# Kernel optimization log

Hardware: AMD Instinct MI355X
Metric: run time of the kernel (lower is better)

The kernel has to match this reference:

```python
import jax, jax.numpy as jnp
import numpy as np

H, W, D = 1024, 1024, 128


def setup_inputs() -> dict:
    key = jax.random.key(0)
    ks = jax.random.split(key, 7)
    x = jax.random.normal(ks[0], (2, H, W), dtype=jnp.float32)
    s1 = 1.0 / np.sqrt(4.0)
    s2 = 1.0 / np.sqrt(float(D))
    W1 = jax.random.uniform(ks[1], (4, D), jnp.float32, -s1, s1)
    b1 = jax.random.uniform(ks[2], (D,), jnp.float32, -s1, s1)
    W2 = jax.random.uniform(ks[3], (D, D), jnp.float32, -s2, s2)
    b2 = jax.random.uniform(ks[4], (D,), jnp.float32, -s2, s2)
    W3 = jax.random.uniform(ks[5], (D, D), jnp.float32, -s2, s2)
    b3 = jax.random.uniform(ks[6], (D,), jnp.float32, -s2, s2)
    return dict(x=x, W1=W1, b1=b1, W2=W2, b2=b2, W3=W3, b3=b3)


def _masked_norm(v, mask):
    # normalize(v) = (v - min) / (max - min), min/max over nonzero pixels only
    big = jnp.float32(1e30)
    vmin = jnp.min(jnp.where(mask, v, big))
    vmax = jnp.max(jnp.where(mask, v, -big))
    return (v - vmin) / (vmax - vmin)


def reference(x, W1, b1, W2, b2, W3, b3):
    x0, x1 = x[0], x[1]                      # real, imag maps [H, W]
    mask = x0 != 0                            # nonzero-context pixels
    w = mask.astype(x.dtype).reshape(-1)      # [H*W] 0/1 weights

    rows = jnp.broadcast_to(jnp.arange(H, dtype=x.dtype)[:, None], (H, W))
    cols = jnp.broadcast_to(jnp.arange(W, dtype=x.dtype)[None, :], (H, W))
    nr = _masked_norm(rows, mask)
    nc = _masked_norm(cols, mask)

    # per-point features [H*W, 4]: (norm row, norm col, real, imag)
    feats = jnp.stack([nr, nc, x0, x1], axis=-1).reshape(-1, 4)

    # fc3(relu(fc2(fc1(.)))) — note: no activation between fc1 and fc2
    h = feats @ W1 + b1                       # [N, 128]
    h = h @ W2 + b2
    h = jax.nn.relu(h)
    out = h @ W3 + b3                         # [N, 128]

    # mean over nonzero points only
    return (w[:, None] * out).sum(0) / w.sum()
```

## Files before the change

### kernel.cpp

```cpp
#include <hip/hip_runtime.h>
#include <climits>

#define HH 1024
#define WW 1024
#define DD 128
#define NPIX (HH * WW)
#define NSB 256
#define NBB 512

#define RMINP 1024
#define RMAXP 1280
#define CMINP 1536
#define CMAXP 1792
#define CNTP  2048
#define PART  8192

__device__ __forceinline__ void d_stats(const float* __restrict__ x0, int blk,
                                        int tid, int* __restrict__ wsi,
                                        int (*sred)[8]) {
    const float4* x4 = (const float4*)(x0) + (size_t)blk * 1024;
    int any0, any1, any2, any3;
    int cmn = INT_MAX, cmx = -1, cnt = 0;
    int c4 = 4 * tid;
    {
        float4 v;
        bool z0, z1, z2, z3;
        #define STAT_K(K, ANY)                                                 \
            v = x4[K * 256 + tid];                                             \
            z0 = v.x != 0.f; z1 = v.y != 0.f; z2 = v.z != 0.f; z3 = v.w != 0.f;\
            ANY = (int)(z0 | z1 | z2 | z3);                                    \
            if (ANY) {                                                         \
                cmn = min(cmn, z0 ? c4 : (z1 ? c4+1 : (z2 ? c4+2 : c4+3)));    \
                cmx = max(cmx, z3 ? c4+3 : (z2 ? c4+2 : (z1 ? c4+1 : c4)));    \
            }                                                                  \
            cnt += (int)z0 + (int)z1 + (int)z2 + (int)z3;
        STAT_K(0, any0) STAT_K(1, any1) STAT_K(2, any2) STAT_K(3, any3)
        #undef STAT_K
    }
    for (int off = 32; off >= 1; off >>= 1) {
        cmn = min(cmn, __shfl_xor(cmn, off, 64));
        cmx = max(cmx, __shfl_xor(cmx, off, 64));
        cnt += __shfl_xor(cnt, off, 64);
        any0 |= __shfl_xor(any0, off, 64);
        any1 |= __shfl_xor(any1, off, 64);
        any2 |= __shfl_xor(any2, off, 64);
        any3 |= __shfl_xor(any3, off, 64);
    }
    int wave = tid >> 6;
    if ((tid & 63) == 0) {
        sred[wave][0] = cmn; sred[wave][1] = cmx; sred[wave][2] = cnt;
        sred[wave][3] = any0; sred[wave][4] = any1;
        sred[wave][5] = any2; sred[wave][6] = any3;
    }
    __syncthreads();
    if (tid == 0) {
        int a = sred[0][0], b = sred[0][1], c = sred[0][2];
        int f0 = sred[0][3], f1 = sred[0][4], f2 = sred[0][5], f3 = sred[0][6];
        for (int w = 1; w < 4; ++w) {
            a = min(a, sred[w][0]); b = max(b, sred[w][1]); c += sred[w][2];
            f0 |= sred[w][3]; f1 |= sred[w][4]; f2 |= sred[w][5]; f3 |= sred[w][6];
        }
        int r0 = blk * 4;
        wsi[RMINP + blk] = f0 ? r0 : (f1 ? r0+1 : (f2 ? r0+2 : (f3 ? r0+3 : INT_MAX)));
        wsi[RMAXP + blk] = f3 ? r0+3 : (f2 ? r0+2 : (f1 ? r0+1 : (f0 ? r0 : -1)));
        wsi[CMINP + blk] = a;
        wsi[CMAXP + blk] = b;
        wsi[CNTP  + blk] = c;
    }
}

__global__ __launch_bounds__(256) void kA(const float* __restrict__ x0,
                                          const float* __restrict__ W1,
                                          const float* __restrict__ b1,
                                          const float* __restrict__ W2,
                                          const float* __restrict__ b2,
                                          const float* __restrict__ b3,
                                          float* __restrict__ out,
                                          float* __restrict__ wsf,
                                          int* __restrict__ wsi) {
    __shared__ int sred[4][8];
    int blk = blockIdx.x, tid = threadIdx.x;
    if (blk < NSB) { d_stats(x0, blk, tid, wsi, sred); return; }
    if (tid < 128) {
        int j = tid;
        float p0 = 0.f, p1 = 0.f, p2 = 0.f, p3 = 0.f, cc = 0.f;
        #pragma unroll 8
        for (int d = 0; d < DD; ++d) {
            float w2 = W2[d * DD + j];
            p0 = fmaf(W1[0 * DD + d], w2, p0);
            p1 = fmaf(W1[1 * DD + d], w2, p1);
            p2 = fmaf(W1[2 * DD + d], w2, p2);
            p3 = fmaf(W1[3 * DD + d], w2, p3);
            cc = fmaf(b1[d],          w2, cc);
        }
        wsf[64 + 0 * DD + j] = p0;
        wsf[64 + 1 * DD + j] = p1;
        wsf[64 + 2 * DD + j] = p2;
        wsf[64 + 3 * DD + j] = p3;
        wsf[576 + j] = cc + b2[j];
        out[j] = b3[j];
    }
}

__global__ __launch_bounds__(256) void kB(const float* __restrict__ x0,
                                          const float* __restrict__ x1,
                                          float* __restrict__ wsf,
                                          const int* __restrict__ wsi) {
    __shared__ float2 sv[2048];
    __shared__ unsigned short lidx[2048];
    __shared__ int   lcnt;
    __shared__ int   sred[4][4];
    __shared__ float fred[128][9];

    int tid = threadIdx.x, blk = blockIdx.x;
    int wv = tid >> 6, lane = tid & 63;

    if (tid == 0) lcnt = 0;

    int rmn = wsi[RMINP + tid], rmx = wsi[RMAXP + tid];
    int cmn = wsi[CMINP + tid], cmx = wsi[CMAXP + tid];
    for (int off = 32; off >= 1; off >>= 1) {
        rmn = min(rmn, __shfl_xor(rmn, off, 64));
        rmx = max(rmx, __shfl_xor(rmx, off, 64));
        cmn = min(cmn, __shfl_xor(cmn, off, 64));
        cmx = max(cmx, __shfl_xor(cmx, off, 64));
    }
    if (lane == 0) {
        sred[wv][0] = rmn; sred[wv][1] = rmx;
        sred[wv][2] = cmn; sred[wv][3] = cmx;
    }
    __syncthreads();
    rmn = min(min(sred[0][0], sred[1][0]), min(sred[2][0], sred[3][0]));
    rmx = max(max(sred[0][1], sred[1][1]), max(sred[2][1], sred[3][1]));
    cmn = min(min(sred[0][2], sred[1][2]), min(sred[2][2], sred[3][2]));
    cmx = max(max(sred[0][3], sred[1][3]), max(sred[2][3], sred[3][3]));

    const float4* x04 = (const float4*)(x0) + (size_t)blk * 512;
    const float4* x14 = (const float4*)(x1) + (size_t)blk * 512;
    float4* sv4 = (float4*)sv;
    #pragma unroll
    for (int k = 0; k < 2; ++k) {
        int i = k * 256 + tid;
        float4 va = x04[i];
        float4 vb = x14[i];
        sv4[2 * i]     = make_float4(va.x, vb.x, va.y, vb.y);
        sv4[2 * i + 1] = make_float4(va.z, vb.z, va.w, vb.w);
        int p4 = 4 * i;
        if (va.x == 0.f) { int p = atomicAdd(&lcnt, 1); lidx[p] = (unsigned short)(p4 + 0); }
        if (va.y == 0.f) { int p = atomicAdd(&lcnt, 1); lidx[p] = (unsigned short)(p4 + 1); }
        if (va.z == 0.f) { int p = atomicAdd(&lcnt, 1); lidx[p] = (unsigned short)(p4 + 2); }
        if (va.w == 0.f) { int p = atomicAdd(&lcnt, 1); lidx[p] = (unsigned short)(p4 + 3); }
    }
    __syncthreads();

    int ft = tid & 31;
    int rg = (tid >> 5) & 1;
    int cq = tid >> 6;
    int row = blk * 2 + rg;
    float rs = 1.0f / (float)(rmx - rmn);
    float cs = 1.0f / (float)(cmx - cmn);

    float M2[4], M3[4], a1v[4], a1x2[4], rb[4], tA[4], tB[4], acc0[4], acc1[4];
    #pragma unroll
    for (int k = 0; k < 4; ++k) {
        int f = ft + 32 * k;
        M2[k] = wsf[64 + 2 * DD + f];
        M3[k] = wsf[64 + 3 * DD + f];
        float a0 = wsf[64 + 0 * DD + f] * rs;
        float a1 = wsf[64 + 1 * DD + f] * cs;
        float cp = wsf[576 + f] - (float)rmn * a0 - (float)cmn * a1;
        rb[k]  = fmaf((float)row, a0, cp);
        a1v[k] = a1;
        tA[k]  = fmaf((float)(cq * 256), a1, rb[k]);
        tB[k]  = tA[k] + a1;
        a1x2[k] = a1 + a1;
        acc0[k] = 0.f; acc1[k] = 0.f;
    }

    const float4* p = sv4 + rg * 512 + cq * 128;
    #pragma unroll 4
    for (int q = 0; q < 128; ++q) {
        float4 v = p[q];
        #pragma unroll
        for (int k = 0; k < 4; ++k) {
            float d0 = fmaf(v.x, M2[k], fmaf(v.y, M3[k], tA[k]));
            float d1 = fmaf(v.z, M2[k], fmaf(v.w, M3[k], tB[k]));
            acc0[k] += fmaxf(d0, 0.f);
            acc1[k] += fmaxf(d1, 0.f);
            tA[k] += a1x2[k];
            tB[k] += a1x2[k];
        }
    }

    int nz = lcnt;
    for (int ii = 0; ii < nz; ++ii) {
        int px = lidx[ii];
        int zr = px >> 10, zc = px & 1023;
        if (zr == rg && (zc >> 8) == cq) {
            float2 v = sv[px];
            #pragma unroll
            for (int k = 0; k < 4; ++k) {
                float tp = fmaf((float)zc, a1v[k], rb[k]);
                acc0[k] -= fmaxf(fmaf(v.x, M2[k], fmaf(v.y, M3[k], tp)), 0.f);
            }
        }
    }

    #pragma unroll
    for (int k = 0; k < 4; ++k)
        fred[ft + 32 * k][rg * 4 + cq] = acc0[k] + acc1[k];
    __syncthreads();
    if (tid < 128) {
        const float* fr = fred[tid];
        float s = ((fr[0] + fr[1]) + (fr[2] + fr[3]))
                + ((fr[4] + fr[5]) + (fr[6] + fr[7]));
        wsf[PART + (size_t)tid * NBB + blk] = s;
    }
}

__global__ __launch_bounds__(256) void kC(const float* __restrict__ wsf,
                                          const int* __restrict__ wsi,
                                          const float* __restrict__ W3,
                                          float* __restrict__ out) {
    __shared__ float sred[4];
    __shared__ int   cred[4];
    __shared__ float mf_sh;
    int f = blockIdx.x, tid = threadIdx.x;
    int wv = tid >> 6, lane = tid & 63;

    int c = wsi[CNTP + tid];
    for (int off = 32; off >= 1; off >>= 1) c += __shfl_xor(c, off, 64);
    if (lane == 0) cred[wv] = c;

    const float* p = wsf + PART + (size_t)f * NBB;
    float S = p[tid] + p[tid + 256];
    for (int off = 32; off >= 1; off >>= 1) S += __shfl_xor(S, off, 64);
    if (lane == 0) sred[wv] = S;
    __syncthreads();
    if (tid == 0) {
        float tot = (sred[0] + sred[1]) + (sred[2] + sred[3]);
        float cnt = (float)(cred[0] + cred[1] + cred[2] + cred[3]);
        mf_sh = tot / cnt;
    }
    __syncthreads();

    if (tid < 128) {
        float mf = mf_sh;
        atomicAdd(&out[tid], mf * W3[f * DD + tid]);
    }
}

extern "C" void kernel_launch(void* const* d_in, const int* in_sizes, int n_in,
                              void* d_out, int out_size, void* d_ws, size_t ws_size,
                              hipStream_t stream) {
    const float* x  = (const float*)d_in[0];
    const float* x0 = x;
    const float* x1 = x + NPIX;
    const float* W1 = (const float*)d_in[1];
    const float* b1 = (const float*)d_in[2];
    const float* W2 = (const float*)d_in[3];
    const float* b2 = (const float*)d_in[4];
    const float* W3 = (const float*)d_in[5];
    const float* b3 = (const float*)d_in[6];
    float* outp = (float*)d_out;
    float* wsf  = (float*)d_ws;
    int*   wsi  = (int*)d_ws;

    hipLaunchKernelGGL(kA, dim3(NSB + 1), dim3(256), 0, stream,
                       x0, W1, b1, W2, b2, b3, outp, wsf, wsi);
    hipLaunchKernelGGL(kB, dim3(NBB), dim3(256), 0, stream, x0, x1, wsf, wsi);
    hipLaunchKernelGGL(kC, dim3(DD), dim3(256), 0, stream, wsf, wsi, W3, outp);
}
```

Before: 32.52 us.

## Split main pass into one row per block and replace atomic output with matvec kernel

The main per-pixel kernel now handles one image row per block instead of two, which doubles the grid so more blocks run on each CU and each block uses half the shared memory. The final stage is split into a per-feature mean kernel and a single-block kernel that computes the W3 matrix-vector product plus bias. This replaces the atomicAdd accumulation and the bias initialisation done in the first kernel. The trade-offs are an extra kernel launch and a serial 128-term dot product per output in one block. The first kernel also now sums W3 into a workspace slot that nothing reads, which is wasted work.

Result: no change. 32.82 us (+0.9%).

```diff
diff --git a/kernel.cpp b/kernel.cpp
--- a/kernel.cpp
+++ b/kernel.cpp
@@ -6,13 +6,14 @@
 #define DD 128
 #define NPIX (HH * WW)
 #define NSB 256
-#define NBB 512
+#define NBB 1024
 
 #define RMINP 1024
 #define RMAXP 1280
 #define CMINP 1536
 #define CMAXP 1792
 #define CNTP  2048
+#define MOFF  704
 #define PART  8192
 
 __device__ __forceinline__ void d_stats(const float* __restrict__ x0, int blk,
@@ -74,8 +75,7 @@
                                           const float* __restrict__ b1,
                                           const float* __restrict__ W2,
                                           const float* __restrict__ b2,
-                                          const float* __restrict__ b3,
-                                          float* __restrict__ out,
+                                          const float* __restrict__ W3,
                                           float* __restrict__ wsf,
                                           int* __restrict__ wsi) {
     __shared__ int sred[4][8];
@@ -98,7 +98,13 @@
         wsf[64 + 2 * DD + j] = p2;
         wsf[64 + 3 * DD + j] = p3;
         wsf[576 + j] = cc + b2[j];
-        out[j] = b3[j];
+    } else {
+        const float4* w34 = (const float4*)W3;
+        float s = 0.f;
+        for (int k = tid - 128; k < DD * DD / 4; k += 128) {
+            float4 t4 = w34[k]; s += t4.x + t4.y + t4.z + t4.w;
+        }
+        wsf[6200 + tid - 128] = s;
     }
 }
 
@@ -106,8 +112,8 @@
                                           const float* __restrict__ x1,
                                           float* __restrict__ wsf,
                                           const int* __restrict__ wsi) {
-    __shared__ float2 sv[2048];
-    __shared__ unsigned short lidx[2048];
+    __shared__ float2 sv[1024];
+    __shared__ unsigned short lidx[1024];
     __shared__ int   lcnt;
     __shared__ int   sred[4][4];
     __shared__ float fred[128][9];
@@ -135,17 +141,15 @@
     cmn = min(min(sred[0][2], sred[1][2]), min(sred[2][2], sred[3][2]));
     cmx = max(max(sred[0][3], sred[1][3]), max(sred[2][3], sred[3][3]));
 
-    const float4* x04 = (const float4*)(x0) + (size_t)blk * 512;
-    const float4* x14 = (const float4*)(x1) + (size_t)blk * 512;
+    const float4* x04 = (const float4*)(x0) + (size_t)blk * 256;
+    const float4* x14 = (const float4*)(x1) + (size_t)blk * 256;
     float4* sv4 = (float4*)sv;
-    #pragma unroll
-    for (int k = 0; k < 2; ++k) {
-        int i = k * 256 + tid;
-        float4 va = x04[i];
-        float4 vb = x14[i];
-        sv4[2 * i]     = make_float4(va.x, vb.x, va.y, vb.y);
-        sv4[2 * i + 1] = make_float4(va.z, vb.z, va.w, vb.w);
-        int p4 = 4 * i;
+    {
+        float4 va = x04[tid];
+        float4 vb = x14[tid];
+        sv4[2 * tid]     = make_float4(va.x, vb.x, va.y, vb.y);
+        sv4[2 * tid + 1] = make_float4(va.z, vb.z, va.w, vb.w);
+        int p4 = 4 * tid;
         if (va.x == 0.f) { int p = atomicAdd(&lcnt, 1); lidx[p] = (unsigned short)(p4 + 0); }
         if (va.y == 0.f) { int p = atomicAdd(&lcnt, 1); lidx[p] = (unsigned short)(p4 + 1); }
         if (va.z == 0.f) { int p = atomicAdd(&lcnt, 1); lidx[p] = (unsigned short)(p4 + 2); }
@@ -154,9 +158,8 @@
     __syncthreads();
 
     int ft = tid & 31;
-    int rg = (tid >> 5) & 1;
-    int cq = tid >> 6;
-    int row = blk * 2 + rg;
+    int cq = tid >> 5;
+    int row = blk;
     float rs = 1.0f / (float)(rmx - rmn);
     float cs = 1.0f / (float)(cmx - cmn);
 
@@ -171,15 +174,15 @@
         float cp = wsf[576 + f] - (float)rmn * a0 - (float)cmn * a1;
         rb[k]  = fmaf((float)row, a0, cp);
         a1v[k] = a1;
-        tA[k]  = fmaf((float)(cq * 256), a1, rb[k]);
+        tA[k]  = fmaf((float)(cq * 128), a1, rb[k]);
         tB[k]  = tA[k] + a1;
         a1x2[k] = a1 + a1;
         acc0[k] = 0.f; acc1[k] = 0.f;
     }
 
-    const float4* p = sv4 + rg * 512 + cq * 128;
+    const float4* p = sv4 + cq * 64;
     #pragma unroll 4
-    for (int q = 0; q < 128; ++q) {
+    for (int q = 0; q < 64; ++q) {
         float4 v = p[q];
         #pragma unroll
         for (int k = 0; k < 4; ++k) {
@@ -195,12 +198,11 @@
     int nz = lcnt;
     for (int ii = 0; ii < nz; ++ii) {
         int px = lidx[ii];
-        int zr = px >> 10, zc = px & 1023;
-        if (zr == rg && (zc >> 8) == cq) {
+        if ((px >> 7) == cq) {
             float2 v = sv[px];
             #pragma unroll
             for (int k = 0; k < 4; ++k) {
-                float tp = fmaf((float)zc, a1v[k], rb[k]);
+                float tp = fmaf((float)px, a1v[k], rb[k]);
                 acc0[k] -= fmaxf(fmaf(v.x, M2[k], fmaf(v.y, M3[k], tp)), 0.f);
             }
         }
@@ -208,7 +210,7 @@
 
     #pragma unroll
     for (int k = 0; k < 4; ++k)
-        fred[ft + 32 * k][rg * 4 + cq] = acc0[k] + acc1[k];
+        fred[ft + 32 * k][cq] = acc0[k] + acc1[k];
     __syncthreads();
     if (tid < 128) {
         const float* fr = fred[tid];
@@ -218,13 +220,10 @@
     }
 }
 
-__global__ __launch_bounds__(256) void kC(const float* __restrict__ wsf,
-                                          const int* __restrict__ wsi,
-                                          const float* __restrict__ W3,
-                                          float* __restrict__ out) {
+__global__ __launch_bounds__(256) void kC1(float* __restrict__ wsf,
+                                           const int* __restrict__ wsi) {
     __shared__ float sred[4];
     __shared__ int   cred[4];
-    __shared__ float mf_sh;
     int f = blockIdx.x, tid = threadIdx.x;
     int wv = tid >> 6, lane = tid & 63;
 
@@ -232,22 +231,37 @@
     for (int off = 32; off >= 1; off >>= 1) c += __shfl_xor(c, off, 64);
     if (lane == 0) cred[wv] = c;
 
-    const float* p = wsf + PART + (size_t)f * NBB;
-    float S = p[tid] + p[tid + 256];
+    const float4* p = (const float4*)(wsf + PART + (size_t)f * NBB);
+    float4 v = p[tid];
+    float S = (v.x + v.y) + (v.z + v.w);
     for (int off = 32; off >= 1; off >>= 1) S += __shfl_xor(S, off, 64);
     if (lane == 0) sred[wv] = S;
     __syncthreads();
     if (tid == 0) {
         float tot = (sred[0] + sred[1]) + (sred[2] + sred[3]);
         float cnt = (float)(cred[0] + cred[1] + cred[2] + cred[3]);
-        mf_sh = tot / cnt;
-    }
-    __syncthreads();
-
-    if (tid < 128) {
-        float mf = mf_sh;
-        atomicAdd(&out[tid], mf * W3[f * DD + tid]);
-    }
+        wsf[MOFF + f] = tot / cnt;
+    }
+}
+
+__global__ __launch_bounds__(256) void kC2(const float* __restrict__ wsf,
+                                           const float* __restrict__ W3,
+                                           const float* __restrict__ b3,
+                                           float* __restrict__ out) {
+    __shared__ float sm[128];
+    __shared__ float s2[256];
+    int tid = threadIdx.x;
+    if (tid < 128) sm[tid] = wsf[MOFF + tid];
+    __syncthreads();
+
+    int col = tid & 127, h = tid >> 7;
+    float o = 0.f;
+    #pragma unroll 8
+    for (int d = h * 64; d < h * 64 + 64; ++d)
+        o = fmaf(sm[d], W3[d * DD + col], o);
+    s2[tid] = o;
+    __syncthreads();
+    if (tid < 128) out[tid] = b3[tid] + s2[tid] + s2[tid + 128];
 }
 
 extern "C" void kernel_launch(void* const* d_in, const int* in_sizes, int n_in,
@@ -267,7 +281,8 @@
     int*   wsi  = (int*)d_ws;
 
     hipLaunchKernelGGL(kA, dim3(NSB + 1), dim3(256), 0, stream,
-                       x0, W1, b1, W2, b2, b3, outp, wsf, wsi);
+                       x0, W1, b1, W2, b2, W3, wsf, wsi);
     hipLaunchKernelGGL(kB, dim3(NBB), dim3(256), 0, stream, x0, x1, wsf, wsi);
-    hipLaunchKernelGGL(kC, dim3(DD), dim3(256), 0, stream, wsf, wsi, W3, outp);
-}
+    hipLaunchKernelGGL(kC1, dim3(DD), dim3(256), 0, stream, wsf, wsi);
+    hipLaunchKernelGGL(kC2, dim3(1), dim3(256), 0, stream, wsf, W3, b3, outp);
+}
```

## Process one row per block with packed f32x2 FMA math in kB

Applied to the files above, without the earlier changes.

Halves the per-block work in kB so each block handles one image row, and the grid grows to 1024 blocks. The shared layout changes so each float4 holds a real pair and an imaginary pair, letting the inner loop use 2-wide vector FMA/max that can map to packed FP32 instructions. kC now reads 1024 partials per feature with float4 loads. The cost is more blocks and more partial sums to reduce.

Result: faster. 31.50 us (-3.2%).

```diff
diff --git a/kernel.cpp b/kernel.cpp
--- a/kernel.cpp
+++ b/kernel.cpp
@@ -6,7 +6,7 @@
 #define DD 128
 #define NPIX (HH * WW)
 #define NSB 256
-#define NBB 512
+#define NBB 1024
 
 #define RMINP 1024
 #define RMAXP 1280
@@ -14,6 +14,8 @@
 #define CMAXP 1792
 #define CNTP  2048
 #define PART  8192
+
+typedef __attribute__((ext_vector_type(2))) float f32x2;
 
 __device__ __forceinline__ void d_stats(const float* __restrict__ x0, int blk,
                                         int tid, int* __restrict__ wsi,
@@ -106,8 +108,8 @@
                                           const float* __restrict__ x1,
                                           float* __restrict__ wsf,
                                           const int* __restrict__ wsi) {
-    __shared__ float2 sv[2048];
-    __shared__ unsigned short lidx[2048];
+    __shared__ float sv_f[4096];
+    __shared__ unsigned short lidx[1024];
     __shared__ int   lcnt;
     __shared__ int   sred[4][4];
     __shared__ float fred[128][9];
@@ -135,17 +137,15 @@
     cmn = min(min(sred[0][2], sred[1][2]), min(sred[2][2], sred[3][2]));
     cmx = max(max(sred[0][3], sred[1][3]), max(sred[2][3], sred[3][3]));
 
-    const float4* x04 = (const float4*)(x0) + (size_t)blk * 512;
-    const float4* x14 = (const float4*)(x1) + (size_t)blk * 512;
-    float4* sv4 = (float4*)sv;
-    #pragma unroll
-    for (int k = 0; k < 2; ++k) {
-        int i = k * 256 + tid;
-        float4 va = x04[i];
-        float4 vb = x14[i];
-        sv4[2 * i]     = make_float4(va.x, vb.x, va.y, vb.y);
-        sv4[2 * i + 1] = make_float4(va.z, vb.z, va.w, vb.w);
-        int p4 = 4 * i;
+    const float4* x04 = (const float4*)(x0) + (size_t)blk * 256;
+    const float4* x14 = (const float4*)(x1) + (size_t)blk * 256;
+    float4* sv4 = (float4*)sv_f;
+    {
+        float4 va = x04[tid];
+        float4 vb = x14[tid];
+        sv4[2 * tid]     = make_float4(va.x, va.y, vb.x, vb.y);
+        sv4[2 * tid + 1] = make_float4(va.z, va.w, vb.z, vb.w);
+        int p4 = 4 * tid;
         if (va.x == 0.f) { int p = atomicAdd(&lcnt, 1); lidx[p] = (unsigned short)(p4 + 0); }
         if (va.y == 0.f) { int p = atomicAdd(&lcnt, 1); lidx[p] = (unsigned short)(p4 + 1); }
         if (va.z == 0.f) { int p = atomicAdd(&lcnt, 1); lidx[p] = (unsigned short)(p4 + 2); }
@@ -154,61 +154,66 @@
     __syncthreads();
 
     int ft = tid & 31;
-    int rg = (tid >> 5) & 1;
-    int cq = tid >> 6;
-    int row = blk * 2 + rg;
+    int cq = tid >> 5;
+    int row = blk;
     float rs = 1.0f / (float)(rmx - rmn);
     float cs = 1.0f / (float)(cmx - cmn);
 
-    float M2[4], M3[4], a1v[4], a1x2[4], rb[4], tA[4], tB[4], acc0[4], acc1[4];
+    f32x2 M2v[4], M3v[4], tv[4], st[4], acc[4];
+    float a1v[4], rb[4];
+    float accsub[4];
     #pragma unroll
     for (int k = 0; k < 4; ++k) {
         int f = ft + 32 * k;
-        M2[k] = wsf[64 + 2 * DD + f];
-        M3[k] = wsf[64 + 3 * DD + f];
+        float M2 = wsf[64 + 2 * DD + f];
+        float M3 = wsf[64 + 3 * DD + f];
         float a0 = wsf[64 + 0 * DD + f] * rs;
         float a1 = wsf[64 + 1 * DD + f] * cs;
         float cp = wsf[576 + f] - (float)rmn * a0 - (float)cmn * a1;
         rb[k]  = fmaf((float)row, a0, cp);
         a1v[k] = a1;
-        tA[k]  = fmaf((float)(cq * 256), a1, rb[k]);
-        tB[k]  = tA[k] + a1;
-        a1x2[k] = a1 + a1;
-        acc0[k] = 0.f; acc1[k] = 0.f;
-    }
-
-    const float4* p = sv4 + rg * 512 + cq * 128;
+        float tA = fmaf((float)(cq * 128), a1, rb[k]);
+        M2v[k] = (f32x2)M2;
+        M3v[k] = (f32x2)M3;
+        tv[k].x = tA; tv[k].y = tA + a1;
+        st[k] = (f32x2)(a1 + a1);
+        acc[k] = (f32x2)0.f;
+        accsub[k] = 0.f;
+    }
+
+    const float4* p = sv4 + cq * 64;
     #pragma unroll 4
-    for (int q = 0; q < 128; ++q) {
+    for (int q = 0; q < 64; ++q) {
         float4 v = p[q];
+        f32x2 v0; v0.x = v.x; v0.y = v.y;
+        f32x2 v1; v1.x = v.z; v1.y = v.w;
         #pragma unroll
         for (int k = 0; k < 4; ++k) {
-            float d0 = fmaf(v.x, M2[k], fmaf(v.y, M3[k], tA[k]));
-            float d1 = fmaf(v.z, M2[k], fmaf(v.w, M3[k], tB[k]));
-            acc0[k] += fmaxf(d0, 0.f);
-            acc1[k] += fmaxf(d1, 0.f);
-            tA[k] += a1x2[k];
-            tB[k] += a1x2[k];
+            f32x2 d = __builtin_elementwise_fma(v0, M2v[k],
+                        __builtin_elementwise_fma(v1, M3v[k], tv[k]));
+            f32x2 r = __builtin_elementwise_max(d, (f32x2)0.f);
+            acc[k] += r;
+            tv[k] += st[k];
         }
     }
 
     int nz = lcnt;
     for (int ii = 0; ii < nz; ++ii) {
         int px = lidx[ii];
-        int zr = px >> 10, zc = px & 1023;
-        if (zr == rg && (zc >> 8) == cq) {
-            float2 v = sv[px];
+        if ((px >> 7) == cq) {
+            float v0 = sv_f[(px >> 1) * 4 + (px & 1)];
+            float v1 = sv_f[(px >> 1) * 4 + 2 + (px & 1)];
             #pragma unroll
             for (int k = 0; k < 4; ++k) {
-                float tp = fmaf((float)zc, a1v[k], rb[k]);
-                acc0[k] -= fmaxf(fmaf(v.x, M2[k], fmaf(v.y, M3[k], tp)), 0.f);
+                float tp = fmaf((float)px, a1v[k], rb[k]);
+                accsub[k] += fmaxf(fmaf(v0, M2v[k].x, fmaf(v1, M3v[k].x, tp)), 0.f);
             }
         }
     }
 
     #pragma unroll
     for (int k = 0; k < 4; ++k)
-        fred[ft + 32 * k][rg * 4 + cq] = acc0[k] + acc1[k];
+        fred[ft + 32 * k][cq] = (acc[k].x + acc[k].y) - accsub[k];
     __syncthreads();
     if (tid < 128) {
         const float* fr = fred[tid];
@@ -232,8 +237,9 @@
     for (int off = 32; off >= 1; off >>= 1) c += __shfl_xor(c, off, 64);
     if (lane == 0) cred[wv] = c;
 
-    const float* p = wsf + PART + (size_t)f * NBB;
-    float S = p[tid] + p[tid + 256];
+    const float4* p = (const float4*)(wsf + PART + (size_t)f * NBB);
+    float4 v = p[tid];
+    float S = (v.x + v.y) + (v.z + v.w);
     for (int off = 32; off >= 1; off >>= 1) S += __shfl_xor(S, off, 64);
     if (lane == 0) sred[wv] = S;
     __syncthreads();
```
